# Kernel optimization log

Hardware: AMD Instinct MI355X
Metric: run time of the kernel (lower is better)

The kernel has to match this reference:

```python
import jax, jax.numpy as jnp
import numpy as np

B, S, D, H = 4, 2048, 1024, 16
HD = D // H  # head_dim = 64


def setup_inputs() -> dict:
    key = jax.random.key(0)
    ks = jax.random.split(key, 6)
    scale = 0.02
    x = jax.random.normal(ks[0], (B, S, D), dtype=jnp.float32)
    # per-head projection weights, torch Linear is y = x @ W.T; store as [H, D, HD]
    Wq = jax.random.normal(ks[1], (H, D, HD), dtype=jnp.float32) * scale
    Wk = jax.random.normal(ks[2], (H, D, HD), dtype=jnp.float32) * scale
    Wv = jax.random.normal(ks[3], (H, D, HD), dtype=jnp.float32) * scale
    Wo = jax.random.normal(ks[4], (D, D), dtype=jnp.float32) * scale  # torch [out, in]
    bo = jax.random.normal(ks[5], (D,), dtype=jnp.float32) * scale
    return {"x": x, "Wq": Wq, "Wk": Wk, "Wv": Wv, "Wo": Wo, "bo": bo}


def reference(x, Wq, Wk, Wv, Wo, bo):
    # project: [B,S,D] x [H,D,HD] -> [B,H,S,HD]
    q = jnp.einsum("bsd,hde->bhse", x, Wq)
    k = jnp.einsum("bsd,hde->bhse", x, Wk)
    v = jnp.einsum("bsd,hde->bhse", x, Wv)
    scores = jnp.einsum("bhse,bhte->bhst", q, k) / jnp.sqrt(jnp.float32(HD))
    causal = jnp.tril(jnp.ones((S, S), dtype=bool))  # same as registered tril mask
    scores = jnp.where(causal, scores, -jnp.inf)
    w = jax.nn.softmax(scores, axis=-1)
    out = jnp.einsum("bhst,bhte->bhse", w, v)  # [B,H,S,HD]
    # concat heads along feature dim: [B,S,H*HD] = [B,S,D]
    out = out.transpose(0, 2, 1, 3).reshape(B, S, D)
    # output projection: torch Linear y = x @ W.T + b
    return jnp.einsum("bsd,od->bso", out, Wo) + bo
```

## Files before the change

### kernel.cpp

```cpp
#include <hip/hip_runtime.h>
#include <hip/hip_bf16.h>

typedef __bf16 bf16x8 __attribute__((ext_vector_type(8)));
typedef float f32x4 __attribute__((ext_vector_type(4)));
typedef unsigned short u16x4 __attribute__((ext_vector_type(4)));
typedef unsigned short u16x8 __attribute__((ext_vector_type(8)));
typedef unsigned uint4v __attribute__((ext_vector_type(4)));

#define B_ 4
#define S_ 2048
#define D_ 1024
#define H_ 16
#define HD_ 64

__device__ __forceinline__ unsigned short f2bf(float f) {
  unsigned u = __float_as_uint(f);
  u += 0x7fff + ((u >> 16) & 1);
  return (unsigned short)(u >> 16);
}

__device__ __forceinline__ void gload16(const void* g, void* l) {
  __builtin_amdgcn_global_load_lds((const __attribute__((address_space(1))) unsigned int*)g,
                                   (__attribute__((address_space(3))) unsigned int*)l,
                                   16, 0, 0);
}

__global__ void pack_x_k(const float* __restrict__ in, unsigned short* __restrict__ out, int n4) {
  int i = blockIdx.x * blockDim.x + threadIdx.x;
  int stride = gridDim.x * blockDim.x;
  for (; i < n4; i += stride) {
    float4 v = reinterpret_cast<const float4*>(in)[i];
    u16x4 o = {f2bf(v.x), f2bf(v.y), f2bf(v.z), f2bf(v.w)};
    reinterpret_cast<u16x4*>(out)[i] = o;
  }
}

__global__ void pack_wqkv_k(const float* __restrict__ Wq, const float* __restrict__ Wk,
                            const float* __restrict__ Wv, unsigned short* __restrict__ Wt) {
  int o = blockIdx.x * blockDim.x + threadIdx.x;
  int n = o >> 10;
  int d = o & 1023;
  const float* W = (n < 1024) ? Wq : (n < 2048) ? Wk : Wv;
  int nn = n & 1023;
  int h = nn >> 6, e = nn & 63;
  Wt[o] = f2bf(W[(h << 16) + (d << 6) + e]);
}

__global__ __launch_bounds__(512, 2) void gemm256_k(const unsigned short* __restrict__ A,
                                                    const unsigned short* __restrict__ Bt,
                                                    unsigned short* __restrict__ C,
                                                    int M, int N, int K) {
  __shared__ __align__(16) unsigned short lds[2][2][2][128 * 64];
  const int tid = threadIdx.x;
  const int wid = tid >> 6, lane = tid & 63;
  const int r = lane & 15, g = lane >> 4;
  const int wm = wid >> 2, wn = wid & 3;

  const int i_hw = blockIdx.y * gridDim.x + blockIdx.x;
  const int xcd = i_hw & 7, j = i_hw >> 3;
  const long arow0 = (long)((xcd & 3) * 8 + (j & 7)) * 256;
  const long bcol0 = (long)((xcd >> 2) * 6 + (j >> 3)) * 256;

  const f32x4 z4 = {0.f, 0.f, 0.f, 0.f};
  f32x4 acc[8][4];
#pragma unroll
  for (int m = 0; m < 8; ++m)
#pragma unroll
    for (int n = 0; n < 4; ++n) acc[m][n] = z4;

  auto stage_half = [&](int kt, int op, int h) {
    const unsigned short* src = op ? Bt + (bcol0 + 128 * h) * K : A + (arow0 + 128 * h) * K;
    const int k0 = kt << 6;
    unsigned short* base = &lds[kt & 1][op][h][0];
#pragma unroll
    for (int c = 0; c < 2; ++c) {
      const int jj = c * 512 + (wid << 6) + lane;
      const int row = jj >> 3, cc = jj & 7;
      const int ccs = cc ^ (row & 7);
      gload16(src + (long)row * K + k0 + ccs * 8, base + (c * 512 + (wid << 6)) * 8);
    }
  };

  bf16x8 af[4][2], bv0[2][2], bv1[2][2];
  auto read_a = [&](int buf, int mh) {
#pragma unroll
    for (int i2 = 0; i2 < 4; ++i2)
#pragma unroll
      for (int kk = 0; kk < 2; ++kk) {
        const int rowh = (2 * i2 + wm) * 16 + r;
        af[i2][kk] = *(const bf16x8*)&lds[buf][0][mh][rowh * 64 + (((kk << 2) + g) ^ (rowh & 7)) * 8];
      }
  };
  auto read_b = [&](bf16x8 (&bv)[2][2], int buf, int nh) {
#pragma unroll
    for (int j2 = 0; j2 < 2; ++j2)
#pragma unroll
      for (int kk = 0; kk < 2; ++kk) {
        const int rowh = (4 * j2 + wn) * 16 + r;
        bv[j2][kk] = *(const bf16x8*)&lds[buf][1][nh][rowh * 64 + (((kk << 2) + g) ^ (rowh & 7)) * 8];
      }
  };
  auto mma_q = [&](bf16x8 (&bv)[2][2], int mh, int nh) {
    __builtin_amdgcn_s_setprio(1);
#pragma unroll
    for (int kk = 0; kk < 2; ++kk)
#pragma unroll
      for (int i2 = 0; i2 < 4; ++i2)
#pragma unroll
        for (int j2 = 0; j2 < 2; ++j2)
          acc[4 * mh + i2][2 * nh + j2] = __builtin_amdgcn_mfma_f32_16x16x32_bf16(
              af[i2][kk], bv[j2][kk], acc[4 * mh + i2][2 * nh + j2], 0, 0, 0);
    __builtin_amdgcn_s_setprio(0);
  };

  const int nk = K >> 6;
  stage_half(0, 0, 0);
  stage_half(0, 1, 0);
  stage_half(0, 1, 1);
  stage_half(0, 0, 1);
  asm volatile("s_waitcnt vmcnt(4)" ::: "memory");
  asm volatile("s_barrier" ::: "memory");

  for (int t = 0; t < nk; ++t) {
    const int buf = t & 1;
    const bool pre = (t + 1 < nk);
    read_a(buf, 0);
    read_b(bv0, buf, 0);
    if (pre) { stage_half(t + 1, 0, 0); stage_half(t + 1, 1, 0); }
    asm volatile("s_barrier" ::: "memory");
    mma_q(bv0, 0, 0);
    if (pre) asm volatile("s_waitcnt vmcnt(6)" ::: "memory");
    else     asm volatile("s_waitcnt vmcnt(2)" ::: "memory");
    asm volatile("s_waitcnt lgkmcnt(0)\n\ts_barrier" ::: "memory");
    read_b(bv1, buf, 1);
    if (pre) stage_half(t + 1, 1, 1);
    asm volatile("s_barrier" ::: "memory");
    mma_q(bv1, 0, 1);
    if (pre) asm volatile("s_waitcnt vmcnt(6)" ::: "memory");
    else     asm volatile("s_waitcnt vmcnt(0)" ::: "memory");
    asm volatile("s_waitcnt lgkmcnt(0)\n\ts_barrier" ::: "memory");
    read_a(buf, 1);
    if (pre) stage_half(t + 1, 0, 1);
    asm volatile("s_barrier" ::: "memory");
    mma_q(bv1, 1, 1);
    asm volatile("s_waitcnt lgkmcnt(0)\n\ts_barrier" ::: "memory");
    asm volatile("s_barrier" ::: "memory");
    mma_q(bv0, 1, 0);
    if (pre) asm volatile("s_waitcnt vmcnt(4)" ::: "memory");
    asm volatile("s_waitcnt lgkmcnt(0)\n\ts_barrier" ::: "memory");
  }

#pragma unroll
  for (int m = 0; m < 8; ++m)
#pragma unroll
    for (int n = 0; n < 4; ++n)
#pragma unroll
      for (int rr = 0; rr < 4; ++rr) {
        const long row = arow0 + (2 * m + wm) * 16 + g * 4 + rr;
        const long col = bcol0 + (4 * n + wn) * 16 + r;
        C[row * N + col] = f2bf(acc[m][n][rr]);
      }
}

__global__ __launch_bounds__(256, 2) void gemm_bt_k(const unsigned short* __restrict__ A,
                                                    const unsigned short* __restrict__ Bt,
                                                    float* __restrict__ C,
                                                    const float* __restrict__ bias,
                                                    int M, int N, int K) {
  __shared__ __align__(16) unsigned short lA[2][128 * 64];
  __shared__ __align__(16) unsigned short lB[2][128 * 64];
  const int tid = threadIdx.x;
  const int wid = tid >> 6, lane = tid & 63;
  const int r = lane & 15, g = lane >> 4;
  const long arow0 = (long)blockIdx.x * 128;
  const long brow0 = (long)blockIdx.y * 128;
  const int wr = (wid >> 1) * 64, wc = (wid & 1) * 64;

  const f32x4 z4 = {0.f, 0.f, 0.f, 0.f};
  f32x4 acc[4][4];
#pragma unroll
  for (int m = 0; m < 4; ++m)
#pragma unroll
    for (int n = 0; n < 4; ++n) acc[m][n] = z4;

  auto stage = [&](int buf, int k0) {
#pragma unroll
    for (int c = 0; c < 4; ++c) {
      const int j = c * 256 + wid * 64 + lane;
      const int row = j >> 3, col = (j & 7) * 8;
      gload16(A + (arow0 + row) * K + k0 + col, &lA[buf][(c * 256 + wid * 64) * 8]);
      gload16(Bt + (brow0 + row) * K + k0 + col, &lB[buf][(c * 256 + wid * 64) * 8]);
    }
  };

  stage(0, 0);
  __syncthreads();
  const int nk = K >> 6;
  for (int kt = 0; kt < nk; ++kt) {
    const int cur = kt & 1;
    if (kt + 1 < nk) stage(cur ^ 1, (kt + 1) << 6);
#pragma unroll
    for (int kk = 0; kk < 2; ++kk) {
      bf16x8 af[4], bfr[4];
#pragma unroll
      for (int m = 0; m < 4; ++m)
        af[m] = *(const bf16x8*)&lA[cur][(wr + m * 16 + r) * 64 + kk * 32 + g * 8];
#pragma unroll
      for (int n = 0; n < 4; ++n)
        bfr[n] = *(const bf16x8*)&lB[cur][(wc + n * 16 + r) * 64 + kk * 32 + g * 8];
#pragma unroll
      for (int m = 0; m < 4; ++m)
#pragma unroll
        for (int n = 0; n < 4; ++n)
          acc[m][n] = __builtin_amdgcn_mfma_f32_16x16x32_bf16(af[m], bfr[n], acc[m][n], 0, 0, 0);
    }
    __syncthreads();
  }

#pragma unroll
  for (int m = 0; m < 4; ++m) {
#pragma unroll
    for (int n = 0; n < 4; ++n) {
#pragma unroll
      for (int rr = 0; rr < 4; ++rr) {
        const long row = arow0 + wr + m * 16 + g * 4 + rr;
        const long col = brow0 + wc + n * 16 + r;
        C[row * N + col] = acc[m][n][rr] + bias[col];
      }
    }
  }
}

__global__ __launch_bounds__(256, 2) void attn_k(const unsigned short* __restrict__ qkv,
                                                 unsigned short* __restrict__ out) {
  __shared__ __align__(16) unsigned short lK[2][64 * 64];
  __shared__ __align__(16) unsigned short lVt[2][64 * 64];

  const int tid = threadIdx.x, wid = tid >> 6, lane = tid & 63;
  const int r = lane & 15, g = lane >> 4;
  const int bh = blockIdx.x;
  const int b = bh >> 4, h = bh & 15;
  const int qb = 15 - (int)blockIdx.y;
  const int q0 = qb * 128;

  const long base = ((long)b * S_) * 3072 + h * 64;
  const unsigned short* Qg = qkv + base;
  const unsigned short* Kg = qkv + base + 1024;
  const unsigned short* Vg = qkv + base + 2048;

  int qrow[2];
  bf16x8 qf[2][2];
#pragma unroll
  for (int qs = 0; qs < 2; ++qs) {
    qrow[qs] = q0 + qs * 64 + wid * 16 + r;
#pragma unroll
    for (int kk = 0; kk < 2; ++kk)
      qf[qs][kk] = *(const bf16x8*)&Qg[(long)qrow[qs] * 3072 + kk * 32 + g * 8];
  }

  const f32x4 z4 = {0.f, 0.f, 0.f, 0.f};
  f32x4 o[2][4];
#pragma unroll
  for (int qs = 0; qs < 2; ++qs)
#pragma unroll
    for (int nt = 0; nt < 4; ++nt) o[qs][nt] = z4;
  float m_i[2] = {-1e30f, -1e30f};
  float l_i[2] = {0.f, 0.f};

  u16x8 kreg[2], vreg[2];
  auto load_regs = [&](int t0) {
#pragma unroll
    for (int c = 0; c < 2; ++c) {
      const int j = c * 256 + tid;
      const int tt = j >> 3, e0 = (j & 7) * 8;
      kreg[c] = *(const u16x8*)&Kg[(long)(t0 + tt) * 3072 + e0];
      const int tc = j & 63, ec = j >> 6;
      vreg[c] = *(const u16x8*)&Vg[(long)(t0 + tc) * 3072 + ec * 8];
    }
  };
  auto write_lds = [&](int buf) {
#pragma unroll
    for (int c = 0; c < 2; ++c) {
      const int j = c * 256 + tid;
      const int row = j >> 3, cc = j & 7;
      *(u16x8*)&lK[buf][(row * 8 + (cc ^ (row & 7))) * 8] = kreg[c];
      const int tc = j & 63, ec = j >> 6;
#pragma unroll
      for (int i = 0; i < 8; ++i) {
        const int e = ec * 8 + i;
        lVt[buf][e * 64 + (tc ^ (i * 8))] = vreg[c][i];
      }
    }
  };

  const int ntiles = (q0 >> 6) + 2;
  load_regs(0);
  write_lds(0);

  for (int t = 0; t < ntiles; ++t) {
    const int cur = t & 1;
    if (t + 1 < ntiles) load_regs((t + 1) << 6);
    __syncthreads();

    const int t0 = t << 6;
    const bool act0 = (t < ntiles - 1);
    const bool diag0 = (t == ntiles - 2);
    const bool diag1 = (t == ntiles - 1);

    f32x4 st[2][4];
#pragma unroll
    for (int tt = 0; tt < 4; ++tt) { st[0][tt] = z4; st[1][tt] = z4; }
    __builtin_amdgcn_s_setprio(1);
#pragma unroll
    for (int kk = 0; kk < 2; ++kk)
#pragma unroll
      for (int tt = 0; tt < 4; ++tt) {
        const int row = tt * 16 + r, cc = kk * 4 + g;
        bf16x8 kf = *(const bf16x8*)&lK[cur][(row * 8 + (cc ^ (row & 7))) * 8];
        st[1][tt] = __builtin_amdgcn_mfma_f32_16x16x32_bf16(kf, qf[1][kk], st[1][tt], 0, 0, 0);
        if (act0)
          st[0][tt] = __builtin_amdgcn_mfma_f32_16x16x32_bf16(kf, qf[0][kk], st[0][tt], 0, 0, 0);
      }
    __builtin_amdgcn_s_setprio(0);

    bf16x8 pf[2][2];
    unsigned corr_bits[2] = {0x3f800000u, 0x3f800000u};
    bool dodef[2] = {true, true};
#pragma unroll
    for (int qs = 0; qs < 2; ++qs) {
      if (qs == 0 && !act0) continue;
      const bool diag = qs ? diag1 : diag0;
      float sv[16];
#pragma unroll
      for (int tt = 0; tt < 4; ++tt)
#pragma unroll
        for (int rg = 0; rg < 4; ++rg) {
          float s = st[qs][tt][rg] * 0.125f;
          if (diag && (t0 + tt * 16 + g * 4 + rg > qrow[qs])) s = -1e30f;
          sv[tt * 4 + rg] = s;
        }
      float h0 = fmaxf(fmaxf(fmaxf(sv[0], sv[1]), fmaxf(sv[2], sv[3])),
                       fmaxf(fmaxf(sv[4], sv[5]), fmaxf(sv[6], sv[7])));
      float h1 = fmaxf(fmaxf(fmaxf(sv[8], sv[9]), fmaxf(sv[10], sv[11])),
                       fmaxf(fmaxf(sv[12], sv[13]), fmaxf(sv[14], sv[15])));
      const float pmax = fmaxf(h0, h1);
      const bool defer = __all(pmax - m_i[qs] <= 8.f);
      float corr = 1.f;
      if (!defer) {
        float mx = fmaxf(pmax, m_i[qs]);
        mx = fmaxf(mx, __shfl_xor(mx, 16, 64));
        mx = fmaxf(mx, __shfl_xor(mx, 32, 64));
        corr = __expf(m_i[qs] - mx);
        m_i[qs] = mx;
      }
      dodef[qs] = defer;
      corr_bits[qs] = __float_as_uint(corr);
      float p[16];
      float rs = 0.f;
#pragma unroll
      for (int i = 0; i < 16; ++i) {
        p[i] = __expf(sv[i] - m_i[qs]);
        rs += p[i];
      }
      rs += __shfl_xor(rs, 16, 64);
      rs += __shfl_xor(rs, 32, 64);
      l_i[qs] = l_i[qs] * corr + rs;
      unsigned cw[4][2];
#pragma unroll
      for (int tt = 0; tt < 4; ++tt)
#pragma unroll
        for (int e = 0; e < 2; ++e)
          asm("v_cvt_pk_bf16_f32 %0, %1, %2"
              : "=v"(cw[tt][e]) : "v"(p[tt * 4 + 2 * e]), "v"(p[tt * 4 + 2 * e + 1]));
#pragma unroll
      for (int kk = 0; kk < 2; ++kk) {
        unsigned x0 = cw[2 * kk][0], y0 = cw[2 * kk + 1][0];
        unsigned x1 = cw[2 * kk][1], y1 = cw[2 * kk + 1][1];
        asm volatile("v_permlane32_swap_b32 %0, %1" : "+v"(x0), "+v"(y0));
        asm volatile("v_permlane16_swap_b32 %0, %1" : "+v"(x0), "+v"(y0));
        asm volatile("v_permlane32_swap_b32 %0, %1" : "+v"(x1), "+v"(y1));
        asm volatile("v_permlane16_swap_b32 %0, %1" : "+v"(x1), "+v"(y1));
        uint4v w = {x0, x1, y0, y1};
        pf[qs][kk] = *(bf16x8*)&w;
      }
    }
#pragma unroll
    for (int qs = 0; qs < 2; ++qs) {
      if (qs == 0 && !act0) continue;
      if (!dodef[qs]) {
        const float corr = __uint_as_float(corr_bits[qs]);
#pragma unroll
        for (int rr = 0; rr < 4; ++rr) {
          const float c = __shfl(corr, g * 4 + rr, 64);
#pragma unroll
          for (int nt = 0; nt < 4; ++nt) o[qs][nt][rr] *= c;
        }
      }
    }

    __builtin_amdgcn_s_setprio(1);
#pragma unroll
    for (int kk = 0; kk < 2; ++kk)
#pragma unroll
      for (int nt = 0; nt < 4; ++nt) {
        const int row = nt * 16 + r, cc = kk * 4 + g;
        const bf16x8 vf = *(const bf16x8*)&lVt[cur][(row * 8 + (cc ^ (row & 7))) * 8];
        o[1][nt] = __builtin_amdgcn_mfma_f32_16x16x32_bf16(pf[1][kk], vf, o[1][nt], 0, 0, 0);
        if (act0)
          o[0][nt] = __builtin_amdgcn_mfma_f32_16x16x32_bf16(pf[0][kk], vf, o[0][nt], 0, 0, 0);
      }
    __builtin_amdgcn_s_setprio(0);

    if (t + 1 < ntiles) write_lds(cur ^ 1);
  }

#pragma unroll
  for (int qs = 0; qs < 2; ++qs) {
    float linv[4];
#pragma unroll
    for (int rr = 0; rr < 4; ++rr)
      linv[rr] = 1.f / __shfl(l_i[qs], g * 4 + rr, 64);
#pragma unroll
    for (int nt = 0; nt < 4; ++nt)
#pragma unroll
      for (int rr = 0; rr < 4; ++rr) {
        const long s = q0 + qs * 64 + wid * 16 + g * 4 + rr;
        out[((long)b * S_ + s) * 1024 + h * 64 + nt * 16 + r] = f2bf(o[qs][nt][rr] * linv[rr]);
      }
  }
}

extern "C" void kernel_launch(void* const* d_in, const int* in_sizes, int n_in,
                              void* d_out, int out_size, void* d_ws, size_t ws_size,
                              hipStream_t stream) {
  const float* x = (const float*)d_in[0];
  const float* Wq = (const float*)d_in[1];
  const float* Wk = (const float*)d_in[2];
  const float* Wv = (const float*)d_in[3];
  const float* Wo = (const float*)d_in[4];
  const float* bo = (const float*)d_in[5];
  float* out = (float*)d_out;

  char* ws = (char*)d_ws;
  unsigned short* Xb = (unsigned short*)(ws);
  unsigned short* Wt = (unsigned short*)(ws + (16ul << 20));
  unsigned short* Wob = (unsigned short*)(ws + (22ul << 20));
  unsigned short* QKV = (unsigned short*)(ws + (24ul << 20));
  unsigned short* AO = (unsigned short*)(ws + (72ul << 20));

  pack_x_k<<<2048, 256, 0, stream>>>(x, Xb, (B_ * S_ * D_) / 4);
  pack_x_k<<<512, 256, 0, stream>>>(Wo, Wob, (D_ * D_) / 4);
  pack_wqkv_k<<<(3 * D_ * D_) / 256, 256, 0, stream>>>(Wq, Wk, Wv, Wt);

  gemm256_k<<<dim3(32, 12), 512, 0, stream>>>(Xb, Wt, QKV, B_ * S_, 3 * D_, D_);
  attn_k<<<dim3(64, 16), 256, 0, stream>>>(QKV, AO);
  gemm_bt_k<<<dim3(64, 8), 256, 0, stream>>>(AO, Wob, out, bo, B_ * S_, D_, D_);
}
```

Baseline: 188.5 us.

## Transpose PV MFMA, compute row sums via ones-MFMA, fold scale into exp2

Swaps the PV MFMA operand order so each lane owns a full query row, which lets the rescale factor apply without per-row shuffles and lets the output be stored as 4-element vector writes. Row sums of P are now accumulated by an extra MFMA against a ones vector instead of a VALU sum plus cross-lane shuffles. The 1/sqrt(d) scale is folded into an exp2 constant applied with FMA. The lazy-rescale threshold is raised to account for the unscaled scores. This trades extra MFMA work for fewer VALU and shuffle instructions in the softmax critical path.

Result: slower. 201.4 us (+6.9%).

```diff
diff --git a/kernel.cpp b/kernel.cpp
--- a/kernel.cpp
+++ b/kernel.cpp
@@ -260,12 +260,16 @@
 
   const f32x4 z4 = {0.f, 0.f, 0.f, 0.f};
   f32x4 o[2][4];
+  f32x4 lacc[2] = {z4, z4};
 #pragma unroll
   for (int qs = 0; qs < 2; ++qs)
 #pragma unroll
     for (int nt = 0; nt < 4; ++nt) o[qs][nt] = z4;
   float m_i[2] = {-1e30f, -1e30f};
-  float l_i[2] = {0.f, 0.f};
+  const float C2 = 0.18033688011112042f;
+
+  uint4v onesw = {0x3F803F80u, 0x3F803F80u, 0x3F803F80u, 0x3F803F80u};
+  const bf16x8 ones = *(const bf16x8*)&onesw;
 
   u16x8 kreg[2], vreg[2];
   auto load_regs = [&](int t0) {
@@ -324,7 +328,7 @@
     __builtin_amdgcn_s_setprio(0);
 
     bf16x8 pf[2][2];
-    unsigned corr_bits[2] = {0x3f800000u, 0x3f800000u};
+    float corr[2] = {1.f, 1.f};
     bool dodef[2] = {true, true};
 #pragma unroll
     for (int qs = 0; qs < 2; ++qs) {
@@ -335,36 +339,28 @@
       for (int tt = 0; tt < 4; ++tt)
 #pragma unroll
         for (int rg = 0; rg < 4; ++rg) {
-          float s = st[qs][tt][rg] * 0.125f;
+          float s = st[qs][tt][rg];
           if (diag && (t0 + tt * 16 + g * 4 + rg > qrow[qs])) s = -1e30f;
           sv[tt * 4 + rg] = s;
         }
-      float h0 = fmaxf(fmaxf(fmaxf(sv[0], sv[1]), fmaxf(sv[2], sv[3])),
-                       fmaxf(fmaxf(sv[4], sv[5]), fmaxf(sv[6], sv[7])));
-      float h1 = fmaxf(fmaxf(fmaxf(sv[8], sv[9]), fmaxf(sv[10], sv[11])),
-                       fmaxf(fmaxf(sv[12], sv[13]), fmaxf(sv[14], sv[15])));
-      const float pmax = fmaxf(h0, h1);
-      const bool defer = __all(pmax - m_i[qs] <= 8.f);
-      float corr = 1.f;
+      const float pmax = fmaxf(
+          fmaxf(fmaxf(fmaxf(sv[0], sv[1]), fmaxf(sv[2], sv[3])),
+                fmaxf(fmaxf(sv[4], sv[5]), fmaxf(sv[6], sv[7]))),
+          fmaxf(fmaxf(fmaxf(sv[8], sv[9]), fmaxf(sv[10], sv[11])),
+                fmaxf(fmaxf(sv[12], sv[13]), fmaxf(sv[14], sv[15]))));
+      const bool defer = __all(pmax - m_i[qs] <= 64.f);
       if (!defer) {
         float mx = fmaxf(pmax, m_i[qs]);
         mx = fmaxf(mx, __shfl_xor(mx, 16, 64));
         mx = fmaxf(mx, __shfl_xor(mx, 32, 64));
-        corr = __expf(m_i[qs] - mx);
+        corr[qs] = exp2f((m_i[qs] - mx) * C2);
         m_i[qs] = mx;
       }
       dodef[qs] = defer;
-      corr_bits[qs] = __float_as_uint(corr);
+      const float m2 = m_i[qs] * C2;
       float p[16];
-      float rs = 0.f;
-#pragma unroll
-      for (int i = 0; i < 16; ++i) {
-        p[i] = __expf(sv[i] - m_i[qs]);
-        rs += p[i];
-      }
-      rs += __shfl_xor(rs, 16, 64);
-      rs += __shfl_xor(rs, 32, 64);
-      l_i[qs] = l_i[qs] * corr + rs;
+#pragma unroll
+      for (int i = 0; i < 16; ++i) p[i] = exp2f(__builtin_fmaf(sv[i], C2, -m2));
       unsigned cw[4][2];
 #pragma unroll
       for (int tt = 0; tt < 4; ++tt)
@@ -388,27 +384,28 @@
     for (int qs = 0; qs < 2; ++qs) {
       if (qs == 0 && !act0) continue;
       if (!dodef[qs]) {
-        const float corr = __uint_as_float(corr_bits[qs]);
-#pragma unroll
-        for (int rr = 0; rr < 4; ++rr) {
-          const float c = __shfl(corr, g * 4 + rr, 64);
-#pragma unroll
-          for (int nt = 0; nt < 4; ++nt) o[qs][nt][rr] *= c;
-        }
+        const float c = corr[qs];
+#pragma unroll
+        for (int nt = 0; nt < 4; ++nt) o[qs][nt] *= c;
+        lacc[qs] *= c;
       }
     }
 
     __builtin_amdgcn_s_setprio(1);
 #pragma unroll
-    for (int kk = 0; kk < 2; ++kk)
+    for (int kk = 0; kk < 2; ++kk) {
 #pragma unroll
       for (int nt = 0; nt < 4; ++nt) {
         const int row = nt * 16 + r, cc = kk * 4 + g;
         const bf16x8 vf = *(const bf16x8*)&lVt[cur][(row * 8 + (cc ^ (row & 7))) * 8];
-        o[1][nt] = __builtin_amdgcn_mfma_f32_16x16x32_bf16(pf[1][kk], vf, o[1][nt], 0, 0, 0);
+        o[1][nt] = __builtin_amdgcn_mfma_f32_16x16x32_bf16(vf, pf[1][kk], o[1][nt], 0, 0, 0);
         if (act0)
-          o[0][nt] = __builtin_amdgcn_mfma_f32_16x16x32_bf16(pf[0][kk], vf, o[0][nt], 0, 0, 0);
-      }
+          o[0][nt] = __builtin_amdgcn_mfma_f32_16x16x32_bf16(vf, pf[0][kk], o[0][nt], 0, 0, 0);
+      }
+      lacc[1] = __builtin_amdgcn_mfma_f32_16x16x32_bf16(ones, pf[1][kk], lacc[1], 0, 0, 0);
+      if (act0)
+        lacc[0] = __builtin_amdgcn_mfma_f32_16x16x32_bf16(ones, pf[0][kk], lacc[0], 0, 0, 0);
+    }
     __builtin_amdgcn_s_setprio(0);
 
     if (t + 1 < ntiles) write_lds(cur ^ 1);
@@ -416,17 +413,15 @@
 
 #pragma unroll
   for (int qs = 0; qs < 2; ++qs) {
-    float linv[4];
-#pragma unroll
-    for (int rr = 0; rr < 4; ++rr)
-      linv[rr] = 1.f / __shfl(l_i[qs], g * 4 + rr, 64);
-#pragma unroll
-    for (int nt = 0; nt < 4; ++nt)
-#pragma unroll
-      for (int rr = 0; rr < 4; ++rr) {
-        const long s = q0 + qs * 64 + wid * 16 + g * 4 + rr;
-        out[((long)b * S_ + s) * 1024 + h * 64 + nt * 16 + r] = f2bf(o[qs][nt][rr] * linv[rr]);
-      }
+    const float linv = 1.f / lacc[qs][0];
+    const long s = q0 + qs * 64 + wid * 16 + r;
+#pragma unroll
+    for (int nt = 0; nt < 4; ++nt) {
+      u16x4 w4;
+#pragma unroll
+      for (int rr = 0; rr < 4; ++rr) w4[rr] = f2bf(o[qs][nt][rr] * linv);
+      *(u16x4*)&out[((long)b * S_ + s) * 1024 + h * 64 + nt * 16 + g * 4] = w4;
+    }
   }
 }
 
```
